# Optimization experiments

Hardware: AMD Instinct MI355X
Metric: run time of the kernel (lower is better)

## Reference

```python
import jax, jax.numpy as jnp
import numpy as np

M, N, K = 35637, 15872, 20
FEAT = 128
EPS = 1e-5
W0 = 1.0  # Sine frequency


def setup_inputs() -> dict:
    key = jax.random.key(0)
    ks = jax.random.split(key, 8)
    x_feat = jax.random.normal(ks[0], (1, N, FEAT), dtype=jnp.float32)
    w_up_inputs = jax.random.uniform(ks[1], (1, 7, M, K), dtype=jnp.float32)
    idx = jax.random.randint(ks[2], (1, M, K), 0, N - 1)
    conv0_w = jax.random.normal(ks[3], (128, 7), dtype=jnp.float32) * (1.0 / np.sqrt(7))
    convs_w = jax.random.normal(ks[4], (7, 128, 128), dtype=jnp.float32) * (1.0 / np.sqrt(128))
    gammas = jnp.ones((8, 128), dtype=jnp.float32)
    betas = jnp.zeros((8, 128), dtype=jnp.float32)
    final_w = jax.random.normal(ks[5], (1, 128), dtype=jnp.float32) * (1.0 / np.sqrt(128))
    final_b = jnp.zeros((1,), dtype=jnp.float32)
    return {"x_feat": x_feat, "w_up_inputs": w_up_inputs, "idx": idx,
            "conv0_w": conv0_w, "convs_w": convs_w, "gammas": gammas,
            "betas": betas, "final_w": final_w, "final_b": final_b}


def _conv_bn_sine(h, W, g, b):
    # 1x1 conv == per-point matmul over channel dim; h: (B, M, K, Cin)
    h = jnp.einsum('bmkc,oc->bmko', h, W)
    # BatchNorm2d in training mode: batch stats over (B, M, K) per channel
    mu = jnp.mean(h, axis=(0, 1, 2))
    var = jnp.var(h, axis=(0, 1, 2))
    h = (h - mu) * jax.lax.rsqrt(var + EPS) * g + b
    return jnp.sin(W0 * h)


def reference(x_feat, w_up_inputs, idx, conv0_w, convs_w, gammas, betas, final_w, final_b):
    # w_up_inputs: (B, 7, M, K) -> channels-last (B, M, K, 7)
    h = jnp.transpose(w_up_inputs, (0, 2, 3, 1))
    h = _conv_bn_sine(h, conv0_w, gammas[0], betas[0])
    for i in range(7):
        h = _conv_bn_sine(h, convs_w[i], gammas[i + 1], betas[i + 1])
    # final 1x1 conv with bias -> logits (B, M, K, 1)
    logits = jnp.einsum('bmkc,oc->bmko', h, final_w) + final_b
    w = jax.nn.softmax(logits, axis=2)  # softmax over K neighbors
    # index_points: gather x_feat[b, idx[b, m, k], :] -> (B, M, K, FEAT)
    gathered = jax.vmap(lambda pts, ix: pts[ix])(x_feat, idx)
    feat_H = jnp.sum(w * gathered, axis=2)  # (B, M, FEAT)
    return feat_H
```

## Files before the change

kernel.cpp:

```cpp
#include <hip/hip_runtime.h>

#define PP 712740
#define MM 35637
#define KK 20
#define NF 15872
#define NTILES 44547
#define NSUPER 11137

typedef _Float16 h16;
typedef __attribute__((ext_vector_type(4))) _Float16 f16x4;
typedef __attribute__((ext_vector_type(8))) _Float16 f16x8;
typedef __attribute__((ext_vector_type(4))) float f32x4;

__global__ __launch_bounds__(256) void k_zero(double* __restrict__ gs) {
  const int t = threadIdx.x;
#pragma unroll
  for (int i = 0; i < 8; ++i) gs[i * 256 + t] = 0.0;
}

__global__ __launch_bounds__(256) void k_layer0(
    const float* __restrict__ up,
    const float* __restrict__ w0,
    h16* __restrict__ z,
    double* __restrict__ gs)
{
  __shared__ float w0s[128 * 7];
  __shared__ double red[4][256];
  const int t = threadIdx.x;
  for (int i = t; i < 128 * 7; i += 256) w0s[i] = w0[i];
  __syncthreads();

  const int w = t >> 6;
  const int lane = t & 63;
  const int ln = lane & 15;
  const int q = lane >> 4;

  float sp[32], qp[32];
#pragma unroll
  for (int i = 0; i < 32; ++i) { sp[i] = 0.f; qp[i] = 0.f; }

  const int gw = blockIdx.x * 4 + w;
  for (int tile = gw; tile < NTILES; tile += gridDim.x * 4) {
    const int p = tile * 16 + ln;
    const bool act = p < PP;
    float u[7];
#pragma unroll
    for (int c7 = 0; c7 < 7; ++c7) u[c7] = act ? up[c7 * PP + p] : 0.f;

#pragma unroll
    for (int ks = 0; ks < 4; ++ks) {
      f16x8 o;
#pragma unroll
      for (int j = 0; j < 8; ++j) {
        const int c = ks * 32 + q * 8 + j;
        float acc = 0.f;
#pragma unroll
        for (int c7 = 0; c7 < 7; ++c7) acc = fmaf(w0s[c * 7 + c7], u[c7], acc);
        o[j] = (h16)acc;
        const int si = ks * 8 + j;
        sp[si] += acc;
        qp[si] = fmaf(acc, acc, qp[si]);
      }
      if (act) *(f16x8*)(z + (size_t)p * 128 + ks * 32 + q * 8) = o;
    }
  }

#pragma unroll
  for (int i = 0; i < 32; ++i) {
#pragma unroll
    for (int d = 1; d < 16; d <<= 1) {
      sp[i] += __shfl_xor(sp[i], d, 64);
      qp[i] += __shfl_xor(qp[i], d, 64);
    }
  }
  if (ln == 0) {
#pragma unroll
    for (int ks = 0; ks < 4; ++ks)
#pragma unroll
      for (int j = 0; j < 8; ++j) {
        const int c = ks * 32 + q * 8 + j;
        red[w][c] = (double)sp[ks * 8 + j];
        red[w][128 + c] = (double)qp[ks * 8 + j];
      }
  }
  __syncthreads();
  double v = red[0][t] + red[1][t] + red[2][t] + red[3][t];
  atomicAdd(&gs[t], v);
}

__global__ __launch_bounds__(256, 3) void k_layer(
    h16* __restrict__ z,
    const double* __restrict__ gsp,
    double* __restrict__ gso,
    const float* __restrict__ W,
    const float* __restrict__ gamma,
    const float* __restrict__ beta)
{
  __shared__ h16 act[2][8192];
  __shared__ double red[256];

  const int t = threadIdx.x;
  const int w = t >> 6;
  const int lane = t & 63;
  const int ln = lane & 15;
  const int q = lane >> 4;
  const int G = (int)gridDim.x;

  float sc[8], sh[8];
  {
    const double n = (double)PP;
    const int cb = (t & 15) * 8;
#pragma unroll
    for (int j = 0; j < 8; ++j) {
      const int c = cb + j;
      const double mu = gsp[c] / n;
      const double var = gsp[128 + c] / n - mu * mu;
      const float rstd = (float)(1.0 / sqrt(var + 1e-5));
      sc[j] = rstd * gamma[c];
      sh[j] = beta[c] - (float)mu * sc[j];
    }
  }

  const int ob = w * 32;
  f16x8 wfr[2][4];
#pragma unroll
  for (int nt = 0; nt < 2; ++nt) {
    const int row_g = ob + (ln >> 2) * 8 + nt * 4 + (ln & 3);
    const float* wrow = W + (size_t)row_g * 128;
#pragma unroll
    for (int ks = 0; ks < 4; ++ks) {
      const float* src = wrow + ks * 32 + q * 8;
      const float4 aa = *(const float4*)src;
      const float4 bb = *(const float4*)(src + 4);
      f16x8 b;
      b[0] = (h16)aa.x; b[1] = (h16)aa.y; b[2] = (h16)aa.z; b[3] = (h16)aa.w;
      b[4] = (h16)bb.x; b[5] = (h16)bb.y; b[6] = (h16)bb.z; b[7] = (h16)bb.w;
      wfr[nt][ks] = b;
    }
  }

  float sp[8], qp[8];
#pragma unroll
  for (int i = 0; i < 8; ++i) { sp[i] = 0.f; qp[i] = 0.f; }

  const size_t roff = (size_t)(t >> 4) * 128 + (size_t)(t & 15) * 8;
  const int wbase = ((t >> 4) * 256 + (t & 15) * 16) ^ (((t >> 4) & 7) << 4);
  int raddr[4];
#pragma unroll
  for (int ks = 0; ks < 4; ++ks)
    raddr[ks] = (ln * 256 + ks * 64 + q * 16) ^ ((ln & 7) << 4);

  int stile = blockIdx.x;
  f16x8 raw[4];
  {
    const h16* src = z + (size_t)stile * 8192 + roff;
#pragma unroll
    for (int s = 0; s < 4; ++s) raw[s] = *(const f16x8*)(src + s * 2048);
  }
  int ib = 0;

  for (; stile < NSUPER; stile += G) {
    char* ab = (char*)(&act[ib][0]);

#pragma unroll
    for (int s = 0; s < 4; ++s) {
      f16x8 av;
#pragma unroll
      for (int j = 0; j < 8; ++j)
        av[j] = (h16)__sinf(fmaf((float)raw[s][j], sc[j], sh[j]));
      *(f16x8*)(ab + (wbase + s * 4096)) = av;
    }

    {
      const int nxt = (stile + G < NSUPER) ? stile + G : NSUPER - 1;
      const h16* src = z + (size_t)nxt * 8192 + roff;
#pragma unroll
      for (int s = 0; s < 4; ++s) raw[s] = *(const f16x8*)(src + s * 2048);
    }

    asm volatile("s_waitcnt lgkmcnt(0)\n\ts_barrier" ::: "memory");

#pragma unroll
    for (int ot = 0; ot < 4; ++ot) {
      f16x8 afr[4];
#pragma unroll
      for (int ks = 0; ks < 4; ++ks)
        afr[ks] = *(const f16x8*)(ab + (ot * 4096 + raddr[ks]));

      f32x4 acc0 = (f32x4){0.f, 0.f, 0.f, 0.f};
      f32x4 acc1 = (f32x4){0.f, 0.f, 0.f, 0.f};
#pragma unroll
      for (int ks = 0; ks < 4; ++ks) {
        acc0 = __builtin_amdgcn_mfma_f32_16x16x32_f16(wfr[0][ks], afr[ks], acc0, 0, 0, 0);
        acc1 = __builtin_amdgcn_mfma_f32_16x16x32_f16(wfr[1][ks], afr[ks], acc1, 0, 0, 0);
      }

      const int p = stile * 64 + ot * 16 + ln;
      if (p < PP) {
        f16x8 o;
        o[0] = (h16)acc0[0]; o[1] = (h16)acc0[1]; o[2] = (h16)acc0[2]; o[3] = (h16)acc0[3];
        o[4] = (h16)acc1[0]; o[5] = (h16)acc1[1]; o[6] = (h16)acc1[2]; o[7] = (h16)acc1[3];
        *(f16x8*)(z + (size_t)p * 128 + ob + q * 8) = o;
#pragma unroll
        for (int r = 0; r < 4; ++r) {
          sp[r]     += acc0[r];
          qp[r]      = fmaf(acc0[r], acc0[r], qp[r]);
          sp[4 + r] += acc1[r];
          qp[4 + r]  = fmaf(acc1[r], acc1[r], qp[4 + r]);
        }
      }
    }
    ib ^= 1;
  }

#pragma unroll
  for (int i = 0; i < 8; ++i) {
#pragma unroll
    for (int d = 1; d < 16; d <<= 1) {
      sp[i] += __shfl_xor(sp[i], d, 64);
      qp[i] += __shfl_xor(qp[i], d, 64);
    }
  }
  if (ln == 0) {
#pragma unroll
    for (int r = 0; r < 4; ++r) {
      const int c = ob + q * 8 + r;
      red[c]           = (double)sp[r];
      red[c + 4]       = (double)sp[4 + r];
      red[128 + c]     = (double)qp[r];
      red[128 + c + 4] = (double)qp[4 + r];
    }
  }
  __syncthreads();
  atomicAdd(&gso[t], red[t]);
}

__global__ __launch_bounds__(256) void k_outf(
    const h16* __restrict__ z,
    const double* __restrict__ gsp,
    const float* __restrict__ gamma,
    const float* __restrict__ beta,
    const float* __restrict__ fw,
    const float* __restrict__ fb,
    const int* __restrict__ idx,
    const float* __restrict__ xf,
    float* __restrict__ out)
{
  const int gw = (int)((blockIdx.x * 256 + threadIdx.x) >> 6);
  const int lane = (int)(threadIdx.x & 63);
  if (gw >= MM) return;
  const int m = gw;
  const int c0 = lane * 2;

  float scv[2], shv[2], fv[2];
#pragma unroll
  for (int j = 0; j < 2; ++j) {
    const int c = c0 + j;
    const double n = (double)PP;
    const double mu = gsp[c] / n;
    const double var = gsp[128 + c] / n - mu * mu;
    const float rstd = (float)(1.0 / sqrt(var + 1e-5));
    scv[j] = rstd * gamma[c];
    shv[j] = beta[c] - (float)mu * scv[j];
    fv[j] = fw[c];
  }
  const float fbv = fb[0];

  float l[KK];
#pragma unroll
  for (int k = 0; k < KK; ++k) {
    const h16* zp = z + (size_t)(m * KK + k) * 128 + c0;
    float part = fv[0] * __sinf(fmaf((float)zp[0], scv[0], shv[0]))
               + fv[1] * __sinf(fmaf((float)zp[1], scv[1], shv[1]));
#pragma unroll
    for (int d = 1; d < 64; d <<= 1) part += __shfl_xor(part, d, 64);
    l[k] = part + fbv;
  }

  float mx = l[0];
#pragma unroll
  for (int k = 1; k < KK; ++k) mx = fmaxf(mx, l[k]);
  float ssum = 0.f;
#pragma unroll
  for (int k = 0; k < KK; ++k) { l[k] = __expf(l[k] - mx); ssum += l[k]; }
  const float inv = 1.f / ssum;

  float a0 = 0.f, a1 = 0.f;
#pragma unroll
  for (int k = 0; k < KK; ++k) {
    const int r = idx[m * KK + k];
    const float wk = l[k] * inv;
    a0 = fmaf(wk, xf[r * 128 + lane], a0);
    a1 = fmaf(wk, xf[r * 128 + 64 + lane], a1);
  }
  out[m * 128 + lane] = a0;
  out[m * 128 + 64 + lane] = a1;
}

__global__ __launch_bounds__(256) void k_out(
    const float* __restrict__ logits,
    const int* __restrict__ idx,
    const float* __restrict__ xf,
    float* __restrict__ out)
{
  const int gw = (int)((blockIdx.x * 256 + threadIdx.x) >> 6);
  const int lane = threadIdx.x & 63;
  if (gw >= MM) return;
  const int m = gw;

  float l[KK];
#pragma unroll
  for (int k = 0; k < KK; ++k) l[k] = logits[m * KK + k];
  float mx = l[0];
#pragma unroll
  for (int k = 1; k < KK; ++k) mx = fmaxf(mx, l[k]);
  float ssum = 0.f;
#pragma unroll
  for (int k = 0; k < KK; ++k) { l[k] = __expf(l[k] - mx); ssum += l[k]; }
  const float inv = 1.f / ssum;

  float a0 = 0.f, a1 = 0.f;
#pragma unroll
  for (int k = 0; k < KK; ++k) {
    const int r = idx[m * KK + k];
    const float wk = l[k] * inv;
    a0 = fmaf(wk, xf[r * 128 + lane], a0);
    a1 = fmaf(wk, xf[r * 128 + 64 + lane], a1);
  }
  out[m * 128 + lane] = a0;
  out[m * 128 + 64 + lane] = a1;
}

__global__ __launch_bounds__(256) void k_chain(
    const float* __restrict__ up,
    const float* __restrict__ w0,
    const float* __restrict__ wc,
    const float* __restrict__ gam,
    const float* __restrict__ bet,
    const double* __restrict__ gs,
    double* __restrict__ gso,
    int jl, int mode,
    const float* __restrict__ fw,
    const float* __restrict__ fb,
    float* __restrict__ logits)
{
  __shared__ float sc_s[8][128], sh_s[8][128];
  __shared__ double bred[4][256];
  const int t = threadIdx.x;
  const int lane = t & 63;

  const int nbn = (mode == 0) ? jl : 8;
  for (int i = t; i < nbn * 128; i += 256) {
    const int L = i >> 7, c = i & 127;
    const double n = (double)PP;
    const double mu = gs[L * 256 + c] / n;
    const double var = gs[L * 256 + 128 + c] / n - mu * mu;
    const float rstd = (float)(1.0 / sqrt(var + 1e-5));
    const float sc = rstd * gam[L * 128 + c];
    sc_s[L][c] = sc;
    sh_s[L][c] = bet[L * 128 + c] - (float)mu * sc;
  }
  __syncthreads();

  double lS0 = 0, lS1 = 0, lQ0 = 0, lQ1 = 0;

  for (int p0 = blockIdx.x * 256; p0 < PP; p0 += gridDim.x * 256) {
    const int p = p0 + t;
    const bool act = p < PP;

    float a[128];
    {
      float u[7];
#pragma unroll
      for (int c = 0; c < 7; ++c) u[c] = act ? up[c * PP + p] : 0.f;
#pragma unroll 1
      for (int och = 0; och < 16; ++och) {
#pragma unroll
        for (int j = 0; j < 8; ++j) {
          float acc = 0.f;
#pragma unroll
          for (int c = 0; c < 7; ++c)
            acc = fmaf(w0[(och * 8 + j) * 7 + c], u[c], acc);
          a[och * 8 + j] = acc;
        }
      }
    }

#pragma unroll 1
    for (int L = 0; L < jl; ++L) {
#pragma unroll
      for (int c = 0; c < 128; ++c)
        a[c] = act ? __sinf(fmaf(a[c], sc_s[L][c], sh_s[L][c])) : 0.f;
      float b[128];
      const float* W = wc + (size_t)L * 128 * 128;
#pragma unroll 1
      for (int och = 0; och < 16; ++och) {
#pragma unroll
        for (int j = 0; j < 8; ++j) {
          float acc = 0.f;
#pragma unroll
          for (int c = 0; c < 128; ++c)
            acc = fmaf(W[(och * 8 + j) * 128 + c], a[c], acc);
          b[och * 8 + j] = acc;
        }
      }
#pragma unroll
      for (int c = 0; c < 128; ++c) a[c] = b[c];
    }

    if (mode == 0) {
#pragma unroll
      for (int o = 0; o < 128; ++o) {
        float s = a[o];
        float qv = a[o] * a[o];
#pragma unroll
        for (int d = 32; d > 0; d >>= 1) {
          s += __shfl_xor(s, d, 64);
          qv += __shfl_xor(qv, d, 64);
        }
        if ((o & 63) == lane) {
          if (o < 64) { lS0 += (double)s; lQ0 += (double)qv; }
          else        { lS1 += (double)s; lQ1 += (double)qv; }
        }
      }
    } else if (act) {
      float acc = fb[0];
#pragma unroll
      for (int c = 0; c < 128; ++c) {
        const float h = fmaf(a[c], sc_s[7][c], sh_s[7][c]);
        acc = fmaf(fw[c], __sinf(h), acc);
      }
      logits[p] = acc;
    }
  }

  if (mode == 0) {
    const int w = t >> 6;
    bred[w][lane]       = lS0;
    bred[w][64 + lane]  = lS1;
    bred[w][128 + lane] = lQ0;
    bred[w][192 + lane] = lQ1;
    __syncthreads();
    double v = bred[0][t] + bred[1][t] + bred[2][t] + bred[3][t];
    atomicAdd(&gso[t], v);
  }
}

extern "C" void kernel_launch(void* const* d_in, const int* in_sizes, int n_in,
                              void* d_out, int out_size, void* d_ws, size_t ws_size,
                              hipStream_t stream) {
  const float* xf  = (const float*)d_in[0];
  const float* up  = (const float*)d_in[1];
  const int*   idx = (const int*)d_in[2];
  const float* w0  = (const float*)d_in[3];
  const float* wc  = (const float*)d_in[4];
  const float* gam = (const float*)d_in[5];
  const float* bet = (const float*)d_in[6];
  const float* fw  = (const float*)d_in[7];
  const float* fb  = (const float*)d_in[8];
  float* out = (float*)d_out;

  char* ws = (char*)d_ws;
  const size_t zb     = (size_t)PP * 128 * sizeof(h16);
  const size_t statsb = 8 * 256 * sizeof(double);
  const size_t logb   = (size_t)PP * sizeof(float);
  const int NB = 1024;
  const int nbo = (MM + 3) / 4;

  if (ws_size >= zb + statsb + logb) {
    h16* z = (h16*)ws;
    double* gs = (double*)(ws + zb);

    k_zero<<<1, 256, 0, stream>>>(gs);
    k_layer0<<<NB, 256, 0, stream>>>(up, w0, z, gs);
    for (int i = 1; i <= 7; ++i) {
      k_layer<<<NB, 256, 0, stream>>>(z,
                                      gs + (size_t)(i - 1) * 256,
                                      gs + (size_t)i * 256,
                                      wc + (size_t)(i - 1) * 128 * 128,
                                      gam + (size_t)(i - 1) * 128,
                                      bet + (size_t)(i - 1) * 128);
    }
    k_outf<<<nbo, 256, 0, stream>>>(z, gs + 7 * 256, gam + 7 * 128,
                                    bet + 7 * 128, fw, fb, idx, xf, out);
  } else {
    double* gs = (double*)ws;
    float* logits = (float*)(ws + statsb);

    k_zero<<<1, 256, 0, stream>>>(gs);
    for (int j = 0; j <= 7; ++j) {
      k_chain<<<NB, 256, 0, stream>>>(up, w0, wc, gam, bet, gs,
                                      gs + (size_t)j * 256, j, 0,
                                      fw, fb, logits);
    }
    k_chain<<<NB, 256, 0, stream>>>(up, w0, wc, gam, bet, gs,
                                    nullptr, 7, 1, fw, fb, logits);
    k_out<<<nbo, 256, 0, stream>>>(logits, idx, xf, out);
  }
}
```

Measured before the change: 827.7 us.

## Stage layer outputs through LDS for coalesced stores and ping-pong activation buffers

Layer outputs from the MFMA accumulators are first written into a swizzled LDS buffer and then stored to global memory as fully coalesced contiguous rows, replacing the old scattered 16-byte stores. Layer 0 gets the same LDS staging, with the activation buffer padded to whole supertiles so the tail needs no bounds checks. When the workspace is large enough, two separate z buffers are used ping-pong so layers do not read and write in place. Occupancy is raised to 4 blocks per SM. The cost is an extra LDS round-trip and barrier per tile, plus double the workspace.

```diff
diff --git a/kernel.cpp b/kernel.cpp
--- a/kernel.cpp
+++ b/kernel.cpp
@@ -6,9 +6,9 @@
 #define NF 15872
 #define NTILES 44547
 #define NSUPER 11137
+#define ZROWS (NSUPER * 64)
 
 typedef _Float16 h16;
-typedef __attribute__((ext_vector_type(4))) _Float16 f16x4;
 typedef __attribute__((ext_vector_type(8))) _Float16 f16x8;
 typedef __attribute__((ext_vector_type(4))) float f32x4;
 
@@ -25,6 +25,7 @@
     double* __restrict__ gs)
 {
   __shared__ float w0s[128 * 7];
+  __shared__ h16 tb[4][2048];
   __shared__ double red[4][256];
   const int t = threadIdx.x;
   for (int i = t; i < 128 * 7; i += 256) w0s[i] = w0[i];
@@ -38,6 +39,8 @@
   float sp[32], qp[32];
 #pragma unroll
   for (int i = 0; i < 32; ++i) { sp[i] = 0.f; qp[i] = 0.f; }
+
+  h16* tbw = &tb[w][0];
 
   const int gw = blockIdx.x * 4 + w;
   for (int tile = gw; tile < NTILES; tile += gridDim.x * 4) {
@@ -56,12 +59,22 @@
         float acc = 0.f;
 #pragma unroll
         for (int c7 = 0; c7 < 7; ++c7) acc = fmaf(w0s[c * 7 + c7], u[c7], acc);
+        if (!act) acc = 0.f;
         o[j] = (h16)acc;
         const int si = ks * 8 + j;
         sp[si] += acc;
         qp[si] = fmaf(acc, acc, qp[si]);
       }
-      if (act) *(f16x8*)(z + (size_t)p * 128 + ks * 32 + q * 8) = o;
+      *(f16x8*)(tbw + ln * 128 + (((ks * 4 + q) ^ (ln & 7)) << 3)) = o;
+    }
+
+#pragma unroll
+    for (int pass = 0; pass < 4; ++pass) {
+      const int c = pass * 64 + lane;
+      const int r = c >> 4;
+      const int k = c & 15;
+      const f16x8 v = *(const f16x8*)(tbw + r * 128 + ((k ^ (r & 7)) << 3));
+      *(f16x8*)(z + (size_t)tile * 2048 + (size_t)c * 8) = v;
     }
   }
 
@@ -88,15 +101,17 @@
   atomicAdd(&gs[t], v);
 }
 
-__global__ __launch_bounds__(256, 3) void k_layer(
-    h16* __restrict__ z,
+__global__ __launch_bounds__(256, 4) void k_layer(
+    const h16* zin,
+    h16* zout,
     const double* __restrict__ gsp,
     double* __restrict__ gso,
     const float* __restrict__ W,
     const float* __restrict__ gamma,
     const float* __restrict__ beta)
 {
-  __shared__ h16 act[2][8192];
+  __shared__ h16 actA[8192];
+  __shared__ h16 actB[8192];
   __shared__ double red[256];
 
   const int t = threadIdx.x;
@@ -144,36 +159,38 @@
   for (int i = 0; i < 8; ++i) { sp[i] = 0.f; qp[i] = 0.f; }
 
   const size_t roff = (size_t)(t >> 4) * 128 + (size_t)(t & 15) * 8;
-  const int wbase = ((t >> 4) * 256 + (t & 15) * 16) ^ (((t >> 4) & 7) << 4);
+  const int wbase = (t >> 4) * 256 + (((t & 15) ^ ((t >> 4) & 7)) << 4);
   int raddr[4];
 #pragma unroll
   for (int ks = 0; ks < 4; ++ks)
-    raddr[ks] = (ln * 256 + ks * 64 + q * 16) ^ ((ln & 7) << 4);
+    raddr[ks] = ln * 256 + (((ks * 4 + q) ^ (ln & 7)) << 4);
+  const int obase = ln * 256 + (((w * 4 + q) ^ (ln & 7)) << 4);
+  const int rbase = (t >> 4) * 256 + (((t & 15) ^ ((t >> 4) & 7)) << 4);
 
   int stile = blockIdx.x;
   f16x8 raw[4];
   {
-    const h16* src = z + (size_t)stile * 8192 + roff;
+    const h16* src = zin + (size_t)stile * 8192 + roff;
 #pragma unroll
     for (int s = 0; s < 4; ++s) raw[s] = *(const f16x8*)(src + s * 2048);
   }
-  int ib = 0;
+
+  char* A = (char*)actA;
+  char* B = (char*)actB;
 
   for (; stile < NSUPER; stile += G) {
-    char* ab = (char*)(&act[ib][0]);
-
 #pragma unroll
     for (int s = 0; s < 4; ++s) {
       f16x8 av;
 #pragma unroll
       for (int j = 0; j < 8; ++j)
         av[j] = (h16)__sinf(fmaf((float)raw[s][j], sc[j], sh[j]));
-      *(f16x8*)(ab + (wbase + s * 4096)) = av;
+      *(f16x8*)(A + (wbase + s * 4096)) = av;
     }
 
     {
       const int nxt = (stile + G < NSUPER) ? stile + G : NSUPER - 1;
-      const h16* src = z + (size_t)nxt * 8192 + roff;
+      const h16* src = zin + (size_t)nxt * 8192 + roff;
 #pragma unroll
       for (int s = 0; s < 4; ++s) raw[s] = *(const f16x8*)(src + s * 2048);
     }
@@ -185,7 +202,7 @@
       f16x8 afr[4];
 #pragma unroll
       for (int ks = 0; ks < 4; ++ks)
-        afr[ks] = *(const f16x8*)(ab + (ot * 4096 + raddr[ks]));
+        afr[ks] = *(const f16x8*)(A + (ot * 4096 + raddr[ks]));
 
       f32x4 acc0 = (f32x4){0.f, 0.f, 0.f, 0.f};
       f32x4 acc1 = (f32x4){0.f, 0.f, 0.f, 0.f};
@@ -197,10 +214,6 @@
 
       const int p = stile * 64 + ot * 16 + ln;
       if (p < PP) {
-        f16x8 o;
-        o[0] = (h16)acc0[0]; o[1] = (h16)acc0[1]; o[2] = (h16)acc0[2]; o[3] = (h16)acc0[3];
-        o[4] = (h16)acc1[0]; o[5] = (h16)acc1[1]; o[6] = (h16)acc1[2]; o[7] = (h16)acc1[3];
-        *(f16x8*)(z + (size_t)p * 128 + ob + q * 8) = o;
 #pragma unroll
         for (int r = 0; r < 4; ++r) {
           sp[r]     += acc0[r];
@@ -209,8 +222,22 @@
           qp[4 + r]  = fmaf(acc1[r], acc1[r], qp[4 + r]);
         }
       }
-    }
-    ib ^= 1;
+      f16x8 o;
+      o[0] = (h16)acc0[0]; o[1] = (h16)acc0[1]; o[2] = (h16)acc0[2]; o[3] = (h16)acc0[3];
+      o[4] = (h16)acc1[0]; o[5] = (h16)acc1[1]; o[6] = (h16)acc1[2]; o[7] = (h16)acc1[3];
+      *(f16x8*)(B + (ot * 4096 + obase)) = o;
+    }
+
+    asm volatile("s_waitcnt lgkmcnt(0)\n\ts_barrier" ::: "memory");
+
+    {
+      const size_t zo = (size_t)stile * 8192;
+#pragma unroll
+      for (int pass = 0; pass < 4; ++pass) {
+        const f16x8 v = *(const f16x8*)(B + (pass * 4096 + rbase));
+        *(f16x8*)(zout + zo + (size_t)pass * 2048 + (size_t)t * 8) = v;
+      }
+    }
   }
 
 #pragma unroll
@@ -461,25 +488,44 @@
   float* out = (float*)d_out;
 
   char* ws = (char*)d_ws;
-  const size_t zb     = (size_t)PP * 128 * sizeof(h16);
+  const size_t zb     = (size_t)ZROWS * 128 * sizeof(h16);
   const size_t statsb = 8 * 256 * sizeof(double);
-  const size_t logb   = (size_t)PP * sizeof(float);
   const int NB = 1024;
   const int nbo = (MM + 3) / 4;
 
-  if (ws_size >= zb + statsb + logb) {
-    h16* z = (h16*)ws;
-    double* gs = (double*)(ws + zb);
+  if (ws_size >= 2 * zb + statsb) {
+    h16* z0 = (h16*)ws;
+    h16* z1 = (h16*)(ws + zb);
+    double* gs = (double*)(ws + 2 * zb);
 
     k_zero<<<1, 256, 0, stream>>>(gs);
-    k_layer0<<<NB, 256, 0, stream>>>(up, w0, z, gs);
+    k_layer0<<<NB, 256, 0, stream>>>(up, w0, z0, gs);
+    h16* cur = z0;
     for (int i = 1; i <= 7; ++i) {
-      k_layer<<<NB, 256, 0, stream>>>(z,
+      h16* nxt = (i & 1) ? z1 : z0;
+      k_layer<<<NB, 256, 0, stream>>>(cur, nxt,
                                       gs + (size_t)(i - 1) * 256,
                                       gs + (size_t)i * 256,
                                       wc + (size_t)(i - 1) * 128 * 128,
                                       gam + (size_t)(i - 1) * 128,
                                       bet + (size_t)(i - 1) * 128);
+      cur = nxt;
+    }
+    k_outf<<<nbo, 256, 0, stream>>>(cur, gs + 7 * 256, gam + 7 * 128,
+                                    bet + 7 * 128, fw, fb, idx, xf, out);
+  } else if (ws_size >= zb + statsb) {
+    h16* z = (h16*)ws;
+    double* gs = (double*)(ws + zb);
+
+    k_zero<<<1, 256, 0, stream>>>(gs);
+    k_layer0<<<NB, 256, 0, stream>>>(up, w0, z, gs);
+    for (int i = 1; i <= 7; ++i) {
+      k_layer<<<NB, 256, 0, stream>>>(z, z,
+                                      gs + (size_t)(i - 1) * 256,
+                                      gs + (size_t)i * 256,
+                                      wc + (size_t)(i - 1) * 128 * 128,
+                                      gam + (size_t)(i - 1) * 128,
+                                      bet + (size_t)(i - 1) * 128);
     }
     k_outf<<<nbo, 256, 0, stream>>>(z, gs + 7 * 256, gam + 7 * 128,
                                     bet + 7 * 128, fw, fb, idx, xf, out);
```

Result: faster. 713.7 us (-13.8%).
